# Kernel optimization log

Hardware: AMD Instinct MI355X
Metric: run time of the kernel (lower is better)

Reference implementation:

```python
import jax, jax.numpy as jnp
import numpy as np

N_NODES = 50000
N_EDGES = 800000
IN_DIM, HID, OUT = 64, 128, 32
BN_EPS = 1e-5


def setup_inputs() -> dict:
    key = jax.random.key(0)
    ks = jax.random.split(key, 24)
    def w(k, shape, fan_in):
        return jax.random.normal(k, shape, dtype=jnp.float32) * (1.0 / np.sqrt(fan_in))
    inp = {
        "x": jax.random.normal(ks[0], (N_NODES, IN_DIM), dtype=jnp.float32),
        "edge_index": jax.random.randint(ks[1], (2, N_EDGES), 0, N_NODES, dtype=jnp.int64),
        # layer 0 GIN MLP: in -> hid -> hid
        "w1_0": w(ks[2], (IN_DIM, HID), IN_DIM), "b1_0": jnp.zeros((HID,), jnp.float32),
        "w2_0": w(ks[3], (HID, HID), HID),       "b2_0": jnp.zeros((HID,), jnp.float32),
        # skip projection for layer 0 (in_dim != hidden_dim -> Linear)
        "skip_w": w(ks[4], (IN_DIM, HID), IN_DIM), "skip_b": jnp.zeros((HID,), jnp.float32),
        # batchnorm params (layers 0 and 1 only)
        "bn_g0": jnp.ones((HID,), jnp.float32), "bn_b0": jnp.zeros((HID,), jnp.float32),
        # layer 1 GIN MLP: hid -> hid -> hid
        "w1_1": w(ks[5], (HID, HID), HID), "b1_1": jnp.zeros((HID,), jnp.float32),
        "w2_1": w(ks[6], (HID, HID), HID), "b2_1": jnp.zeros((HID,), jnp.float32),
        "bn_g1": jnp.ones((HID,), jnp.float32), "bn_b1": jnp.zeros((HID,), jnp.float32),
        # layer 2 GIN MLP: hid -> hid -> out
        "w1_2": w(ks[7], (HID, HID), HID), "b1_2": jnp.zeros((HID,), jnp.float32),
        "w2_2": w(ks[8], (HID, OUT), HID), "b2_2": jnp.zeros((OUT,), jnp.float32),
    }
    return inp


def _gin_conv(h, src, dst, n, W1, b1, W2, b2):
    # GINConv (eps=0): mlp((1+eps)*x_i + sum_{j in N(i)} x_j)
    agg = jax.ops.segment_sum(h[src], dst, num_segments=n)  # [N, d]
    z = h + agg
    return jax.nn.relu(z @ W1 + b1) @ W2 + b2


def _bn(h, g, b):
    # training-mode batchnorm over nodes (batch statistics, biased var)
    m = h.mean(0)
    v = jnp.mean((h - m) ** 2, axis=0)
    return g * (h - m) * jax.lax.rsqrt(v + BN_EPS) + b


def reference(x, edge_index, w1_0, b1_0, w2_0, b2_0, skip_w, skip_b, bn_g0, bn_b0,
              w1_1, b1_1, w2_1, b2_1, bn_g1, bn_b1, w1_2, b1_2, w2_2, b2_2):
    src, dst = edge_index[0], edge_index[1]
    n = x.shape[0]
    # layer 0: conv -> bn -> +skip_proj(residual) -> relu (dropout = identity in eval)
    h = _gin_conv(x, src, dst, n, w1_0, b1_0, w2_0, b2_0)
    h = _bn(h, bn_g0, bn_b0)
    h = h + (x @ skip_w + skip_b)
    residual = h
    h = jax.nn.relu(h)
    # layer 1: conv -> bn -> +residual (Identity skip) -> relu
    h = _gin_conv(h, src, dst, n, w1_1, b1_1, w2_1, b2_1)
    h = _bn(h, bn_g1, bn_b1)
    h = h + residual
    h = jax.nn.relu(h)
    # layer 2: conv only (no bn since i >= len(bns), no skip/relu since i == num_layers-1)
    h = _gin_conv(h, src, dst, n, w1_2, b1_2, w2_2, b2_2)
    return h
```

## Files before the change

kernel.cpp:

```cpp
#include <hip/hip_runtime.h>
#include <hip/hip_bf16.h>


#define HID 128
#define NPART 8
#define ABLK 256
#define BBLK 128

typedef __attribute__((ext_vector_type(8))) __bf16 bf16x8;
typedef __attribute__((ext_vector_type(4))) float f32x4;

__device__ __forceinline__ ushort f2b(float f) {
    uint u = __builtin_bit_cast(uint, f);
    u = (u + 0x7fffu + ((u >> 16) & 1u)) >> 16;
    return (ushort)u;
}
__device__ __forceinline__ float b2f(ushort s) {
    return __builtin_bit_cast(float, (uint)s << 16);
}
__device__ __forceinline__ float lo16(uint u) { return __builtin_bit_cast(float, u << 16); }
__device__ __forceinline__ float hi16(uint u) { return __builtin_bit_cast(float, u & 0xffff0000u); }
__device__ __forceinline__ uint packbf(float a, float b) {
    return (uint)f2b(a) | ((uint)f2b(b) << 16);
}

__launch_bounds__(256)
__global__ void ecount_kernel(const int* __restrict__ ei, int* __restrict__ bc,
                              int E, int pchunk) {
    __shared__ int cnt[NPART];
    if (threadIdx.x < NPART) cnt[threadIdx.x] = 0;
    __syncthreads();
    const int epb = (E + ABLK - 1) / ABLK;
    const int e0 = blockIdx.x * epb, e1 = min(e0 + epb, E);
    for (int e = e0 + threadIdx.x; e < e1; e += 256) {
        int d = ei[E + e];
        atomicAdd(&cnt[d / pchunk], 1);
    }
    __syncthreads();
    if (threadIdx.x < NPART) bc[threadIdx.x * ABLK + blockIdx.x] = cnt[threadIdx.x];
}

__launch_bounds__(1024)
__global__ void escan_kernel(int* __restrict__ bc) {
    __shared__ int ls[1024];
    const int t = threadIdx.x;
    const int v0 = bc[2 * t], v1 = bc[2 * t + 1];
    ls[t] = v0 + v1;
    __syncthreads();
    for (int off = 1; off < 1024; off <<= 1) {
        int tmp = (t >= off) ? ls[t - off] : 0;
        __syncthreads();
        ls[t] += tmp;
        __syncthreads();
    }
    const int excl = ls[t] - (v0 + v1);
    bc[2 * t] = excl;
    bc[2 * t + 1] = excl + v0;
}

__launch_bounds__(256)
__global__ void edist_kernel(const int* __restrict__ ei, const int* __restrict__ bc,
                             int2* __restrict__ ebuf, int E, int pchunk) {
    __shared__ int base[NPART];
    if (threadIdx.x < NPART) base[threadIdx.x] = bc[threadIdx.x * ABLK + blockIdx.x];
    __syncthreads();
    const int epb = (E + ABLK - 1) / ABLK;
    const int e0 = blockIdx.x * epb, e1 = min(e0 + epb, E);
    for (int e = e0 + threadIdx.x; e < e1; e += 256) {
        int s = ei[e], d = ei[E + e];
        int pos = atomicAdd(&base[d / pchunk], 1);
        ebuf[pos] = make_int2(s, d);
    }
}

__launch_bounds__(256)
__global__ void histp_kernel(const int2* __restrict__ ebuf, const int* __restrict__ bc,
                             int* __restrict__ deg, int E) {
    const int part = blockIdx.x & (NPART - 1);
    const int blk  = blockIdx.x >> 3;
    const int pstart = bc[part * ABLK];
    const int pend = (part == NPART - 1) ? E : bc[(part + 1) * ABLK];
    const int epb = (pend - pstart + BBLK - 1) / BBLK;
    const int e0 = pstart + blk * epb, e1 = min(e0 + epb, pend);
    for (int e = e0 + threadIdx.x; e < e1; e += 256)
        atomicAdd(&deg[ebuf[e].y], 1);
}

__launch_bounds__(256)
__global__ void scatterp_kernel(const int2* __restrict__ ebuf, const int* __restrict__ bc,
                                int* __restrict__ cursor, int* __restrict__ csr_src, int E) {
    const int part = blockIdx.x & (NPART - 1);
    const int blk  = blockIdx.x >> 3;
    const int pstart = bc[part * ABLK];
    const int pend = (part == NPART - 1) ? E : bc[(part + 1) * ABLK];
    const int epb = (pend - pstart + BBLK - 1) / BBLK;
    const int e0 = pstart + blk * epb, e1 = min(e0 + epb, pend);
    for (int e = e0 + threadIdx.x; e < e1; e += 256) {
        int2 ed = ebuf[e];
        int p = atomicAdd(&cursor[ed.y], 1);
        csr_src[p] = ed.x;
    }
}

__launch_bounds__(256)
__global__ void bsum_kernel(const int* __restrict__ deg, int* __restrict__ bsum, int n) {
    __shared__ int ls[256];
    const int tid = threadIdx.x;
    const int i = blockIdx.x * 256 + tid;
    ls[tid] = (i < n) ? deg[i] : 0;
    __syncthreads();
    for (int off = 128; off > 0; off >>= 1) {
        if (tid < off) ls[tid] += ls[tid + off];
        __syncthreads();
    }
    if (tid == 0) bsum[blockIdx.x] = ls[0];
}

__launch_bounds__(1024)
__global__ void bscan_kernel(int* __restrict__ bsum, int nb) {
    __shared__ int ls[1024];
    const int tid = threadIdx.x;
    const int v = (tid < nb) ? bsum[tid] : 0;
    ls[tid] = v;
    __syncthreads();
    for (int off = 1; off < 1024; off <<= 1) {
        int t = (tid >= off) ? ls[tid - off] : 0;
        __syncthreads();
        ls[tid] += t;
        __syncthreads();
    }
    if (tid < nb) bsum[tid] = ls[tid] - v;
}

__launch_bounds__(256)
__global__ void lscan_kernel(const int* __restrict__ bsum, int* __restrict__ cursor,
                             int* __restrict__ rowptr, int n) {
    __shared__ int ls[256];
    const int tid = threadIdx.x;
    const int i = blockIdx.x * 256 + tid;
    const int v = (i < n) ? cursor[i] : 0;
    ls[tid] = v;
    __syncthreads();
    for (int off = 1; off < 256; off <<= 1) {
        int t = (tid >= off) ? ls[tid - off] : 0;
        __syncthreads();
        ls[tid] += t;
        __syncthreads();
    }
    if (i < n) {
        const int incl = ls[tid] + bsum[blockIdx.x];
        cursor[i] = incl - v;
        rowptr[i + 1] = incl;
        if (i == 0) rowptr[0] = 0;
    }
}

struct PrepAll {
    const float* src[7];
    ushort* dst[7];
    int K[7];
    int N[7];
    int off[8];
};

__launch_bounds__(256)
__global__ void wprep_kernel(PrepAll a) {
    const int b = blockIdx.x;
    int m = 0;
    while (m < 6 && b >= a.off[m + 1]) m++;
    const int K = a.K[m], N = a.N[m];
    const int e = (b - a.off[m]) * 256 + threadIdx.x;
    if (e >= K * N) return;
    const int n = e / K, k = e % K;
    a.dst[m][e] = f2b(a.src[m][(size_t)k * N + n]);
}

__global__ void x2bf_kernel(const float* __restrict__ x, ushort* __restrict__ xb,
                            float* __restrict__ bn0, float* __restrict__ bn1,
                            int* __restrict__ cursor, int n, int total4) {
    if (blockIdx.x == 0 && threadIdx.x < 256) {
        bn0[threadIdx.x] = 0.f;
        bn1[threadIdx.x] = 0.f;
    }
    int i = blockIdx.x * 256 + threadIdx.x;
    if (i < n) cursor[i] = 0;
    if (i < total4) {
        float4 v = reinterpret_cast<const float4*>(x)[i];
        ushort4 o;
        o.x = f2b(v.x); o.y = f2b(v.y); o.z = f2b(v.z); o.w = f2b(v.w);
        reinterpret_cast<ushort4*>(xb)[i] = o;
    }
}

template <int K1, int NC2, bool SKIP, bool OUTBF, bool STATS>
__launch_bounds__(512)
__global__ void fused_layer(const ushort* __restrict__ table,
                            const int* __restrict__ rowptr, const int* __restrict__ csr,
                            const ushort* __restrict__ W1t, const float* __restrict__ b1,
                            const ushort* __restrict__ W2t, const float* __restrict__ b2,
                            float* __restrict__ convf, ushort* __restrict__ convb,
                            const ushort* __restrict__ skw, const float* __restrict__ skb,
                            float* __restrict__ skipout, float* __restrict__ bnsums,
                            int M) {
    __shared__ ushort Zt[64 * K1];
    __shared__ ushort Yt[64 * 128];
    __shared__ float bnloc[256];
    const int tid = threadIdx.x;
    const int w = tid >> 6, lane = tid & 63;
    const int rb0 = blockIdx.x * 64;
    constexpr int ZROWB = K1 * 2;

    if (STATS && tid < 256) bnloc[tid] = 0.f;

    if constexpr (K1 == 128) {
        const uint* t2 = reinterpret_cast<const uint*>(table);
#pragma unroll
        for (int i = 0; i < 8; i++) {
            const int rt = w * 8 + i;
            const int nd = min(rb0 + rt, M - 1);
            const int s = rowptr[nd], e = rowptr[nd + 1];
            uint v = t2[(size_t)nd * 64 + lane];
            float ax = lo16(v), ay = hi16(v);
            for (int k = s; k < e; k += 8) {
                uint uu[8];
#pragma unroll
                for (int j = 0; j < 8; j++)
                    uu[j] = t2[(size_t)csr[min(k + j, e - 1)] * 64 + lane];
#pragma unroll
                for (int j = 0; j < 8; j++) {
                    if (k + j < e) { ax += lo16(uu[j]); ay += hi16(uu[j]); }
                }
            }
            *reinterpret_cast<uint*>(reinterpret_cast<char*>(Zt) +
                (((uint)(rt * 256 + lane * 4)) ^ ((rt & 7) << 4))) = packbf(ax, ay);
        }
    } else {
        const uint* t2 = reinterpret_cast<const uint*>(table);
        const int half = lane >> 5, li = lane & 31;
#pragma unroll
        for (int i = 0; i < 4; i++) {
            const int rt = w * 8 + i * 2 + half;
            const int nd = min(rb0 + rt, M - 1);
            const int s = rowptr[nd], e = rowptr[nd + 1];
            uint v = t2[(size_t)nd * 32 + li];
            float ax = lo16(v), ay = hi16(v);
            for (int k = s; k < e; k += 8) {
                uint uu[8];
#pragma unroll
                for (int j = 0; j < 8; j++)
                    uu[j] = t2[(size_t)csr[min(k + j, e - 1)] * 32 + li];
#pragma unroll
                for (int j = 0; j < 8; j++) {
                    if (k + j < e) { ax += lo16(uu[j]); ay += hi16(uu[j]); }
                }
            }
            *reinterpret_cast<uint*>(reinterpret_cast<char*>(Zt) +
                (((uint)(rt * 128 + li * 4)) ^ ((rt & 7) << 4))) = packbf(ax, ay);
        }
    }
    __syncthreads();

    const int wr = w >> 2, wc = w & 3;
    const int lr = lane & 15, hg = lane >> 4;
    const int xorv = (lr & 7) << 4;

    {
        f32x4 a00 = {}, a01 = {}, a10 = {}, a11 = {};
#pragma unroll
        for (int k0 = 0; k0 < K1; k0 += 32) {
            const uint o0 = (uint)((wr * 32 + lr) * ZROWB + k0 * 2 + hg * 16) ^ xorv;
            const uint o1 = (uint)((wr * 32 + 16 + lr) * ZROWB + k0 * 2 + hg * 16) ^ xorv;
            bf16x8 za0 = *reinterpret_cast<const bf16x8*>(reinterpret_cast<const char*>(Zt) + o0);
            bf16x8 za1 = *reinterpret_cast<const bf16x8*>(reinterpret_cast<const char*>(Zt) + o1);
            bf16x8 wb0 = *reinterpret_cast<const bf16x8*>(W1t + (size_t)(wc * 32 + lr) * K1 + k0 + hg * 8);
            bf16x8 wb1 = *reinterpret_cast<const bf16x8*>(W1t + (size_t)(wc * 32 + 16 + lr) * K1 + k0 + hg * 8);
            a00 = __builtin_amdgcn_mfma_f32_16x16x32_bf16(za0, wb0, a00, 0, 0, 0);
            a01 = __builtin_amdgcn_mfma_f32_16x16x32_bf16(za0, wb1, a01, 0, 0, 0);
            a10 = __builtin_amdgcn_mfma_f32_16x16x32_bf16(za1, wb0, a10, 0, 0, 0);
            a11 = __builtin_amdgcn_mfma_f32_16x16x32_bf16(za1, wb1, a11, 0, 0, 0);
        }
        const int c0 = wc * 32 + lr, c1 = wc * 32 + 16 + lr;
        const float bv0 = b1[c0], bv1 = b1[c1];
        f32x4 accs[2][2] = {{a00, a01}, {a10, a11}};
#pragma unroll
        for (int m = 0; m < 2; m++) {
#pragma unroll
            for (int j = 0; j < 4; j++) {
                const int row = wr * 32 + m * 16 + hg * 4 + j;
                const uint sw = (uint)((row & 7) << 4);
                *reinterpret_cast<ushort*>(reinterpret_cast<char*>(Yt) + ((uint)(row * 256 + c0 * 2) ^ sw)) =
                    f2b(fmaxf(accs[m][0][j] + bv0, 0.f));
                *reinterpret_cast<ushort*>(reinterpret_cast<char*>(Yt) + ((uint)(row * 256 + c1 * 2) ^ sw)) =
                    f2b(fmaxf(accs[m][1][j] + bv1, 0.f));
            }
        }
    }
    __syncthreads();

    if constexpr (SKIP) {
        const uint* x2 = reinterpret_cast<const uint*>(table);
#pragma unroll
        for (int pp = 0; pp < 4; pp++) {
            const int rt = pp * 16 + (tid >> 5);
            const int cu = tid & 31;
            const int nd = min(rb0 + rt, M - 1);
            uint v = x2[(size_t)nd * 32 + cu];
            const uint boff = (uint)(rt * 128 + cu * 4) ^ ((rt & 7) << 4);
            *reinterpret_cast<uint*>(reinterpret_cast<char*>(Zt) + boff) = v;
        }
    }

    if (NC2 == 128 || w < 2) {
        const int wr2 = (NC2 == 128) ? wr : w;
        const int cb2 = (NC2 == 128) ? wc * 32 : 0;
        f32x4 d00 = {}, d01 = {}, d10 = {}, d11 = {};
#pragma unroll
        for (int k0 = 0; k0 < 128; k0 += 32) {
            const uint o0 = (uint)((wr2 * 32 + lr) * 256 + k0 * 2 + hg * 16) ^ xorv;
            const uint o1 = (uint)((wr2 * 32 + 16 + lr) * 256 + k0 * 2 + hg * 16) ^ xorv;
            bf16x8 ya0 = *reinterpret_cast<const bf16x8*>(reinterpret_cast<const char*>(Yt) + o0);
            bf16x8 ya1 = *reinterpret_cast<const bf16x8*>(reinterpret_cast<const char*>(Yt) + o1);
            bf16x8 wb0 = *reinterpret_cast<const bf16x8*>(W2t + (size_t)(cb2 + lr) * 128 + k0 + hg * 8);
            bf16x8 wb1 = *reinterpret_cast<const bf16x8*>(W2t + (size_t)(cb2 + 16 + lr) * 128 + k0 + hg * 8);
            d00 = __builtin_amdgcn_mfma_f32_16x16x32_bf16(ya0, wb0, d00, 0, 0, 0);
            d01 = __builtin_amdgcn_mfma_f32_16x16x32_bf16(ya0, wb1, d01, 0, 0, 0);
            d10 = __builtin_amdgcn_mfma_f32_16x16x32_bf16(ya1, wb0, d10, 0, 0, 0);
            d11 = __builtin_amdgcn_mfma_f32_16x16x32_bf16(ya1, wb1, d11, 0, 0, 0);
        }
        const int c0 = cb2 + lr, c1 = cb2 + 16 + lr;
        const float bv0 = b2[c0], bv1 = b2[c1];
        f32x4 accs[2][2] = {{d00, d01}, {d10, d11}};
        float s0 = 0.f, q0 = 0.f, s1 = 0.f, q1 = 0.f;
#pragma unroll
        for (int m = 0; m < 2; m++) {
#pragma unroll
            for (int j = 0; j < 4; j++) {
                const int row = rb0 + wr2 * 32 + m * 16 + hg * 4 + j;
                if (row < M) {
                    const float v0 = accs[m][0][j] + bv0;
                    const float v1 = accs[m][1][j] + bv1;
                    if (STATS) {
                        s0 += v0; q0 += v0 * v0;
                        s1 += v1; q1 += v1 * v1;
                    }
                    if constexpr (OUTBF) {
                        convb[(size_t)row * NC2 + c0] = f2b(v0);
                        convb[(size_t)row * NC2 + c1] = f2b(v1);
                    } else {
                        convf[(size_t)row * NC2 + c0] = v0;
                        convf[(size_t)row * NC2 + c1] = v1;
                    }
                }
            }
        }
        if (STATS) {
            atomicAdd(&bnloc[c0], s0);
            atomicAdd(&bnloc[c1], s1);
            atomicAdd(&bnloc[128 + c0], q0);
            atomicAdd(&bnloc[128 + c1], q1);
        }
    }

    if constexpr (SKIP) {
        __syncthreads();
        f32x4 s00 = {}, s01 = {}, s10 = {}, s11 = {};
#pragma unroll
        for (int k0 = 0; k0 < 64; k0 += 32) {
            const uint o0 = (uint)((wr * 32 + lr) * 128 + k0 * 2 + hg * 16) ^ xorv;
            const uint o1 = (uint)((wr * 32 + 16 + lr) * 128 + k0 * 2 + hg * 16) ^ xorv;
            bf16x8 za0 = *reinterpret_cast<const bf16x8*>(reinterpret_cast<const char*>(Zt) + o0);
            bf16x8 za1 = *reinterpret_cast<const bf16x8*>(reinterpret_cast<const char*>(Zt) + o1);
            bf16x8 wb0 = *reinterpret_cast<const bf16x8*>(skw + (size_t)(wc * 32 + lr) * 64 + k0 + hg * 8);
            bf16x8 wb1 = *reinterpret_cast<const bf16x8*>(skw + (size_t)(wc * 32 + 16 + lr) * 64 + k0 + hg * 8);
            s00 = __builtin_amdgcn_mfma_f32_16x16x32_bf16(za0, wb0, s00, 0, 0, 0);
            s01 = __builtin_amdgcn_mfma_f32_16x16x32_bf16(za0, wb1, s01, 0, 0, 0);
            s10 = __builtin_amdgcn_mfma_f32_16x16x32_bf16(za1, wb0, s10, 0, 0, 0);
            s11 = __builtin_amdgcn_mfma_f32_16x16x32_bf16(za1, wb1, s11, 0, 0, 0);
        }
        const int c0 = wc * 32 + lr, c1 = wc * 32 + 16 + lr;
        const float bv0 = skb[c0], bv1 = skb[c1];
        f32x4 accs[2][2] = {{s00, s01}, {s10, s11}};
#pragma unroll
        for (int m = 0; m < 2; m++) {
#pragma unroll
            for (int j = 0; j < 4; j++) {
                const int row = rb0 + wr * 32 + m * 16 + hg * 4 + j;
                if (row < M) {
                    skipout[(size_t)row * 128 + c0] = accs[m][0][j] + bv0;
                    skipout[(size_t)row * 128 + c1] = accs[m][1][j] + bv1;
                }
            }
        }
    }

    if constexpr (STATS) {
        __syncthreads();
        if (tid < 256) atomicAdd(&bnsums[tid], bnloc[tid]);
    }
}

template <bool WRITE_RES>
__global__ void bn_apply_kernel(const ushort* __restrict__ conv, const float* __restrict__ sums,
                                const float* __restrict__ gamma, const float* __restrict__ beta,
                                const float* __restrict__ add, float* __restrict__ resf,
                                ushort* __restrict__ outb, int total2, int n) {
    int i = blockIdx.x * blockDim.x + threadIdx.x;
    if (i >= total2) return;
    const int c0 = (i & 63) * 2, c1 = c0 + 1;
    const float inv = 1.f / (float)n;
    const float m0 = sums[c0] * inv, m1 = sums[c1] * inv;
    const float v0 = sums[128 + c0] * inv - m0 * m0;
    const float v1 = sums[128 + c1] * inv - m1 * m1;
    const float sc0 = gamma[c0] * rsqrtf(v0 + 1e-5f);
    const float sc1 = gamma[c1] * rsqrtf(v1 + 1e-5f);
    const uint u = reinterpret_cast<const uint*>(conv)[i];
    const float2 ad = reinterpret_cast<const float2*>(add)[i];
    const float val0 = (lo16(u) - m0) * sc0 + beta[c0] + ad.x;
    const float val1 = (hi16(u) - m1) * sc1 + beta[c1] + ad.y;
    if (WRITE_RES) reinterpret_cast<float2*>(resf)[i] = make_float2(val0, val1);
    reinterpret_cast<uint*>(outb)[i] = packbf(fmaxf(val0, 0.f), fmaxf(val1, 0.f));
}

extern "C" void kernel_launch(void* const* d_in, const int* in_sizes, int n_in,
                              void* d_out, int out_size, void* d_ws, size_t ws_size,
                              hipStream_t stream) {
    const float* x      = (const float*)d_in[0];
    const int*   ei     = (const int*)d_in[1];
    const float* w1_0   = (const float*)d_in[2];
    const float* b1_0   = (const float*)d_in[3];
    const float* w2_0   = (const float*)d_in[4];
    const float* b2_0   = (const float*)d_in[5];
    const float* skip_w = (const float*)d_in[6];
    const float* skip_b = (const float*)d_in[7];
    const float* bn_g0  = (const float*)d_in[8];
    const float* bn_b0  = (const float*)d_in[9];
    const float* w1_1   = (const float*)d_in[10];
    const float* b1_1   = (const float*)d_in[11];
    const float* w2_1   = (const float*)d_in[12];
    const float* b2_1   = (const float*)d_in[13];
    const float* bn_g1  = (const float*)d_in[14];
    const float* bn_b1  = (const float*)d_in[15];
    const float* w1_2   = (const float*)d_in[16];
    const float* b1_2   = (const float*)d_in[17];
    const float* w2_2   = (const float*)d_in[18];
    const float* b2_2   = (const float*)d_in[19];

    const int N = in_sizes[0] / 64;
    const int E = in_sizes[1] / 2;
    const int pchunk = (N + NPART - 1) / NPART;

    char* p = (char*)d_ws;
    auto carve = [&](size_t bytes) -> void* {
        void* q = (void*)p;
        p += (bytes + 255) & ~(size_t)255;
        return q;
    };
    int*   cursor = (int*)carve((size_t)N * 4);
    int*   rowptr = (int*)carve((size_t)(N + 1) * 4);
    int*   csr    = (int*)carve((size_t)E * 4);
    int*   bsum   = (int*)carve(1024 * 4);
    int*   bc     = (int*)carve((size_t)NPART * ABLK * 4);
    int2*  ebuf   = (int2*)carve((size_t)E * 8);
    float* bnsums0 = (float*)carve(256 * 4);
    float* bnsums1 = (float*)carve(256 * 4);
    ushort* w1_0t = (ushort*)carve(64 * 128 * 2);
    ushort* w2_0t = (ushort*)carve(128 * 128 * 2);
    ushort* skwt  = (ushort*)carve(64 * 128 * 2);
    ushort* w1_1t = (ushort*)carve(128 * 128 * 2);
    ushort* w2_1t = (ushort*)carve(128 * 128 * 2);
    ushort* w1_2t = (ushort*)carve(128 * 128 * 2);
    ushort* w2_2t = (ushort*)carve(128 * 32 * 2);
    ushort* x_bf  = (ushort*)carve((size_t)N * 64 * 2);
    ushort* aggin = (ushort*)carve((size_t)N * HID * 2);
    ushort* convB = (ushort*)carve((size_t)N * HID * 2);
    float* bufC_f = (float*)carve((size_t)N * HID * 4);

    const int NB  = (N + 255) / 256;
    const int EWB2 = (N * 64 + 255) / 256;
    const int FUSE_G = (N + 63) / 64;

    PrepAll pa;
    pa.src[0] = w1_0; pa.dst[0] = w1_0t; pa.K[0] = 64;  pa.N[0] = 128;
    pa.src[1] = w2_0; pa.dst[1] = w2_0t; pa.K[1] = 128; pa.N[1] = 128;
    pa.src[2] = skip_w; pa.dst[2] = skwt; pa.K[2] = 64; pa.N[2] = 128;
    pa.src[3] = w1_1; pa.dst[3] = w1_1t; pa.K[3] = 128; pa.N[3] = 128;
    pa.src[4] = w2_1; pa.dst[4] = w2_1t; pa.K[4] = 128; pa.N[4] = 128;
    pa.src[5] = w1_2; pa.dst[5] = w1_2t; pa.K[5] = 128; pa.N[5] = 128;
    pa.src[6] = w2_2; pa.dst[6] = w2_2t; pa.K[6] = 128; pa.N[6] = 32;
    int off = 0;
    for (int m = 0; m < 7; m++) { pa.off[m] = off; off += (pa.K[m] * pa.N[m]) / 256; }
    pa.off[7] = off;
    wprep_kernel<<<off, 256, 0, stream>>>(pa);
    x2bf_kernel<<<(N * 64 / 4 + 255) / 256, 256, 0, stream>>>(x, x_bf, bnsums0, bnsums1, cursor, N, N * 64 / 4);

    ecount_kernel<<<ABLK, 256, 0, stream>>>(ei, bc, E, pchunk);
    escan_kernel<<<1, 1024, 0, stream>>>(bc);
    edist_kernel<<<ABLK, 256, 0, stream>>>(ei, bc, ebuf, E, pchunk);
    histp_kernel<<<NPART * BBLK, 256, 0, stream>>>(ebuf, bc, cursor, E);
    bsum_kernel<<<NB, 256, 0, stream>>>(cursor, bsum, N);
    bscan_kernel<<<1, 1024, 0, stream>>>(bsum, NB);
    lscan_kernel<<<NB, 256, 0, stream>>>(bsum, cursor, rowptr, N);
    scatterp_kernel<<<NPART * BBLK, 256, 0, stream>>>(ebuf, bc, cursor, csr, E);

    fused_layer<64, 128, true, true, true><<<FUSE_G, 512, 0, stream>>>(
        x_bf, rowptr, csr, w1_0t, b1_0, w2_0t, b2_0, nullptr, convB, skwt, skip_b, bufC_f, bnsums0, N);
    bn_apply_kernel<true><<<EWB2, 256, 0, stream>>>(convB, bnsums0, bn_g0, bn_b0, bufC_f, bufC_f, aggin, N * 64, N);

    fused_layer<128, 128, false, true, true><<<FUSE_G, 512, 0, stream>>>(
        aggin, rowptr, csr, w1_1t, b1_1, w2_1t, b2_1, nullptr, convB, nullptr, nullptr, nullptr, bnsums1, N);
    bn_apply_kernel<false><<<EWB2, 256, 0, stream>>>(convB, bnsums1, bn_g1, bn_b1, bufC_f, nullptr, aggin, N * 64, N);

    fused_layer<128, 32, false, false, false><<<FUSE_G, 512, 0, stream>>>(
        aggin, rowptr, csr, w1_2t, b1_2, w2_2t, b2_2, (float*)d_out, nullptr, nullptr, nullptr, nullptr, nullptr, N);
}
```

Baseline: 329.7 us.

## Pad CSR rows to multiples of eight with zero-row sentinel, shard BN atomics

Each CSR row is padded to a multiple of 8 entries, and the padding slots point at an extra zero-valued row appended to the bf16 feature tables. This removes the min/bounds checks in the gather loop so it can issue unconditional loads. BatchNorm partial sums are also spread across 8 copies, chosen by block index, to reduce atomic contention; the apply kernel sums those copies. The cost is extra padded gathers (up to 7 per node) and more memory for the CSR.

```diff
diff --git a/kernel.cpp b/kernel.cpp
--- a/kernel.cpp
+++ b/kernel.cpp
@@ -107,7 +107,7 @@
     __shared__ int ls[256];
     const int tid = threadIdx.x;
     const int i = blockIdx.x * 256 + tid;
-    ls[tid] = (i < n) ? deg[i] : 0;
+    ls[tid] = (i < n) ? ((deg[i] + 7) & ~7) : 0;
     __syncthreads();
     for (int off = 128; off > 0; off >>= 1) {
         if (tid < off) ls[tid] += ls[tid + off];
@@ -134,12 +134,13 @@
 
 __launch_bounds__(256)
 __global__ void lscan_kernel(const int* __restrict__ bsum, int* __restrict__ cursor,
-                             int* __restrict__ rowptr, int n) {
+                             int* __restrict__ rowptr, int* __restrict__ csr, int n) {
     __shared__ int ls[256];
     const int tid = threadIdx.x;
     const int i = blockIdx.x * 256 + tid;
     const int v = (i < n) ? cursor[i] : 0;
-    ls[tid] = v;
+    const int vp = (v + 7) & ~7;
+    ls[tid] = vp;
     __syncthreads();
     for (int off = 1; off < 256; off <<= 1) {
         int t = (tid >= off) ? ls[tid - off] : 0;
@@ -149,9 +150,11 @@
     }
     if (i < n) {
         const int incl = ls[tid] + bsum[blockIdx.x];
-        cursor[i] = incl - v;
+        const int excl = incl - vp;
+        cursor[i] = excl;
         rowptr[i + 1] = incl;
         if (i == 0) rowptr[0] = 0;
+        for (int q = excl + v; q < incl; q++) csr[q] = n;
     }
 }
 
@@ -177,18 +180,20 @@
 
 __global__ void x2bf_kernel(const float* __restrict__ x, ushort* __restrict__ xb,
                             float* __restrict__ bn0, float* __restrict__ bn1,
-                            int* __restrict__ cursor, int n, int total4) {
-    if (blockIdx.x == 0 && threadIdx.x < 256) {
-        bn0[threadIdx.x] = 0.f;
-        bn1[threadIdx.x] = 0.f;
-    }
-    int i = blockIdx.x * 256 + threadIdx.x;
-    if (i < n) cursor[i] = 0;
-    if (i < total4) {
-        float4 v = reinterpret_cast<const float4*>(x)[i];
+                            int* __restrict__ cursor, uint* __restrict__ xb_sent,
+                            uint* __restrict__ agg_sent, int n, int total4) {
+    const int gi = blockIdx.x * 256 + threadIdx.x;
+    if (gi < 2048) { bn0[gi] = 0.f; bn1[gi] = 0.f; }
+    if (blockIdx.x == 0) {
+        if (threadIdx.x < 64) agg_sent[threadIdx.x] = 0;
+        else if (threadIdx.x < 96) xb_sent[threadIdx.x - 64] = 0;
+    }
+    if (gi < n) cursor[gi] = 0;
+    if (gi < total4) {
+        float4 v = reinterpret_cast<const float4*>(x)[gi];
         ushort4 o;
         o.x = f2b(v.x); o.y = f2b(v.y); o.z = f2b(v.z); o.w = f2b(v.w);
-        reinterpret_cast<ushort4*>(xb)[i] = o;
+        reinterpret_cast<ushort4*>(xb)[gi] = o;
     }
 }
 
@@ -204,7 +209,7 @@
                             int M) {
     __shared__ ushort Zt[64 * K1];
     __shared__ ushort Yt[64 * 128];
-    __shared__ float bnloc[256];
+    __shared__ float bnloc[STATS ? 256 : 1];
     const int tid = threadIdx.x;
     const int w = tid >> 6, lane = tid & 63;
     const int rb0 = blockIdx.x * 64;
@@ -222,13 +227,11 @@
             uint v = t2[(size_t)nd * 64 + lane];
             float ax = lo16(v), ay = hi16(v);
             for (int k = s; k < e; k += 8) {
-                uint uu[8];
-#pragma unroll
-                for (int j = 0; j < 8; j++)
-                    uu[j] = t2[(size_t)csr[min(k + j, e - 1)] * 64 + lane];
 #pragma unroll
                 for (int j = 0; j < 8; j++) {
-                    if (k + j < e) { ax += lo16(uu[j]); ay += hi16(uu[j]); }
+                    uint u = t2[(size_t)csr[k + j] * 64 + lane];
+                    ax += lo16(u);
+                    ay += hi16(u);
                 }
             }
             *reinterpret_cast<uint*>(reinterpret_cast<char*>(Zt) +
@@ -245,13 +248,11 @@
             uint v = t2[(size_t)nd * 32 + li];
             float ax = lo16(v), ay = hi16(v);
             for (int k = s; k < e; k += 8) {
-                uint uu[8];
-#pragma unroll
-                for (int j = 0; j < 8; j++)
-                    uu[j] = t2[(size_t)csr[min(k + j, e - 1)] * 32 + li];
 #pragma unroll
                 for (int j = 0; j < 8; j++) {
-                    if (k + j < e) { ax += lo16(uu[j]); ay += hi16(uu[j]); }
+                    uint u = t2[(size_t)csr[k + j] * 32 + li];
+                    ax += lo16(u);
+                    ay += hi16(u);
                 }
             }
             *reinterpret_cast<uint*>(reinterpret_cast<char*>(Zt) +
@@ -395,7 +396,7 @@
 
     if constexpr (STATS) {
         __syncthreads();
-        if (tid < 256) atomicAdd(&bnsums[tid], bnloc[tid]);
+        if (tid < 256) atomicAdd(&bnsums[((blockIdx.x & 7) << 8) + tid], bnloc[tid]);
     }
 }
 
@@ -407,10 +408,17 @@
     int i = blockIdx.x * blockDim.x + threadIdx.x;
     if (i >= total2) return;
     const int c0 = (i & 63) * 2, c1 = c0 + 1;
+    float S0 = 0.f, S1 = 0.f, Q0 = 0.f, Q1 = 0.f;
+#pragma unroll
+    for (int b = 0; b < 8; b++) {
+        const float* bp = sums + (b << 8);
+        S0 += bp[c0]; S1 += bp[c1];
+        Q0 += bp[128 + c0]; Q1 += bp[128 + c1];
+    }
     const float inv = 1.f / (float)n;
-    const float m0 = sums[c0] * inv, m1 = sums[c1] * inv;
-    const float v0 = sums[128 + c0] * inv - m0 * m0;
-    const float v1 = sums[128 + c1] * inv - m1 * m1;
+    const float m0 = S0 * inv, m1 = S1 * inv;
+    const float v0 = Q0 * inv - m0 * m0;
+    const float v1 = Q1 * inv - m1 * m1;
     const float sc0 = gamma[c0] * rsqrtf(v0 + 1e-5f);
     const float sc1 = gamma[c1] * rsqrtf(v1 + 1e-5f);
     const uint u = reinterpret_cast<const uint*>(conv)[i];
@@ -457,12 +465,12 @@
     };
     int*   cursor = (int*)carve((size_t)N * 4);
     int*   rowptr = (int*)carve((size_t)(N + 1) * 4);
-    int*   csr    = (int*)carve((size_t)E * 4);
+    int*   csr    = (int*)carve((size_t)(E + 8 * (size_t)N + 8) * 4);
     int*   bsum   = (int*)carve(1024 * 4);
     int*   bc     = (int*)carve((size_t)NPART * ABLK * 4);
     int2*  ebuf   = (int2*)carve((size_t)E * 8);
-    float* bnsums0 = (float*)carve(256 * 4);
-    float* bnsums1 = (float*)carve(256 * 4);
+    float* bnsums0 = (float*)carve(2048 * 4);
+    float* bnsums1 = (float*)carve(2048 * 4);
     ushort* w1_0t = (ushort*)carve(64 * 128 * 2);
     ushort* w2_0t = (ushort*)carve(128 * 128 * 2);
     ushort* skwt  = (ushort*)carve(64 * 128 * 2);
@@ -470,8 +478,8 @@
     ushort* w2_1t = (ushort*)carve(128 * 128 * 2);
     ushort* w1_2t = (ushort*)carve(128 * 128 * 2);
     ushort* w2_2t = (ushort*)carve(128 * 32 * 2);
-    ushort* x_bf  = (ushort*)carve((size_t)N * 64 * 2);
-    ushort* aggin = (ushort*)carve((size_t)N * HID * 2);
+    ushort* x_bf  = (ushort*)carve((size_t)(N + 1) * 64 * 2);
+    ushort* aggin = (ushort*)carve((size_t)(N + 1) * HID * 2);
     ushort* convB = (ushort*)carve((size_t)N * HID * 2);
     float* bufC_f = (float*)carve((size_t)N * HID * 4);
 
@@ -491,7 +499,10 @@
     for (int m = 0; m < 7; m++) { pa.off[m] = off; off += (pa.K[m] * pa.N[m]) / 256; }
     pa.off[7] = off;
     wprep_kernel<<<off, 256, 0, stream>>>(pa);
-    x2bf_kernel<<<(N * 64 / 4 + 255) / 256, 256, 0, stream>>>(x, x_bf, bnsums0, bnsums1, cursor, N, N * 64 / 4);
+    x2bf_kernel<<<(N * 64 / 4 + 255) / 256, 256, 0, stream>>>(
+        x, x_bf, bnsums0, bnsums1, cursor,
+        reinterpret_cast<uint*>(x_bf + (size_t)N * 64),
+        reinterpret_cast<uint*>(aggin + (size_t)N * HID), N, N * 64 / 4);
 
     ecount_kernel<<<ABLK, 256, 0, stream>>>(ei, bc, E, pchunk);
     escan_kernel<<<1, 1024, 0, stream>>>(bc);
@@ -499,7 +510,7 @@
     histp_kernel<<<NPART * BBLK, 256, 0, stream>>>(ebuf, bc, cursor, E);
     bsum_kernel<<<NB, 256, 0, stream>>>(cursor, bsum, N);
     bscan_kernel<<<1, 1024, 0, stream>>>(bsum, NB);
-    lscan_kernel<<<NB, 256, 0, stream>>>(bsum, cursor, rowptr, N);
+    lscan_kernel<<<NB, 256, 0, stream>>>(bsum, cursor, rowptr, csr, N);
     scatterp_kernel<<<NPART * BBLK, 256, 0, stream>>>(ebuf, bc, cursor, csr, E);
 
     fused_layer<64, 128, true, true, true><<<FUSE_G, 512, 0, stream>>>(
```

Result: faster. 305.6 us (-7.3%).
